# Optimization experiments

Measured on AMD Instinct MI355X. Metric: run time of the kernel, lower is better.

The kernel has to match this reference:

```python
import jax, jax.numpy as jnp
import numpy as np

N_HEADS = 16

def setup_inputs() -> dict:
    key = jax.random.key(0)
    k1, k2 = jax.random.split(key)
    B, S, H = 4, 2048, 1024
    hidden_states = jax.random.normal(k1, (B, S, H), dtype=jnp.float32)
    # F.linear weight: [out_features, in_features]; init std per module
    std = 0.02 / np.sqrt(2.0 * 24 * H)
    queries_weight = jax.random.normal(k2, (H, H), dtype=jnp.float32) * std
    return {"hidden_states": hidden_states, "queries_weight": queries_weight}


def reference(hidden_states, queries_weight):
    B, S, H = hidden_states.shape
    hd = H // N_HEADS
    # F.linear: x @ W^T
    q = hidden_states @ queries_weight.T
    qh = q.reshape(B, S, N_HEADS, hd)          # [B,S,h,d]
    xh = hidden_states.reshape(B, S, N_HEADS, hd)
    # pre_attn = Q K^T (no softmax), then attn @ V with K=V=x heads
    pre_attn = jnp.einsum('bqhd,bkhd->bhqk', qh, xh)   # [B,h,S,S]
    attn = jnp.einsum('bhqk,bkhd->bqhd', pre_attn, xh) # [B,S,h,d]
    return attn.reshape(B, S, H)
```

## Files before the change

### kernel.cpp

```cpp
#include <hip/hip_runtime.h>
#include <hip/hip_bf16.h>


typedef __bf16 bf16x8 __attribute__((ext_vector_type(8)));
typedef float f32x4 __attribute__((ext_vector_type(4)));

typedef __attribute__((address_space(3))) unsigned int lds_u32;
typedef const __attribute__((address_space(1))) unsigned int glb_u32;

__device__ __forceinline__ void gld_lds16(const void* g, void* l) {
    __builtin_amdgcn_global_load_lds((glb_u32*)g, (lds_u32*)l, 16, 0, 0);
}

__device__ __forceinline__ unsigned short f2bf(float f) {
    unsigned int u = __float_as_uint(f);
    u += 0x7FFFu + ((u >> 16) & 1u);
    return (unsigned short)(u >> 16);
}

#define XT_S 136

__global__ __launch_bounds__(256) void gx_partial(
        const float* __restrict__ x, const float* __restrict__ W,
        unsigned short* __restrict__ xb, unsigned short* __restrict__ Wb,
        float* __restrict__ Gp) {
    __shared__ __align__(16) unsigned short xt[64 * XT_S];
    const int tid = threadIdx.x;
    const int chunk = blockIdx.x;
    const int bh = blockIdx.y;
    const int fb = bh * 8 + chunk;
    const int b = bh >> 4, h = bh & 15;
    const int wave = tid >> 6, lane = tid & 63;
    const int lm = lane & 15, quad = lane >> 4;

    {
        size_t base = (size_t)fb * 2048 + (size_t)tid * 8;
        float4 v0 = *(const float4*)&W[base];
        float4 v1 = *(const float4*)&W[base + 4];
        ushort4 o0 = {f2bf(v0.x), f2bf(v0.y), f2bf(v0.z), f2bf(v0.w)};
        ushort4 o1 = {f2bf(v1.x), f2bf(v1.y), f2bf(v1.z), f2bf(v1.w)};
        *(ushort4*)&Wb[base] = o0;
        *(ushort4*)&Wb[base + 4] = o1;
    }

    f32x4 acc[4] = {};
    for (int half = 0; half < 2; ++half) {
        const size_t gbase =
            ((size_t)(b * 2048 + chunk * 256 + half * 128)) * 1024 + h * 64;
        __syncthreads();
        #pragma unroll
        for (int i = 0; i < 8; ++i) {
            int idx = tid + 256 * i;
            int s = idx >> 4;
            int c = (idx & 15) * 4;
            float4 v = *(const float4*)&x[gbase + (size_t)s * 1024 + c];
            ushort4 o = {f2bf(v.x), f2bf(v.y), f2bf(v.z), f2bf(v.w)};
            *(ushort4*)&xb[gbase + (size_t)s * 1024 + c] = o;
            xt[(c + 0) * XT_S + s] = o.x;
            xt[(c + 1) * XT_S + s] = o.y;
            xt[(c + 2) * XT_S + s] = o.z;
            xt[(c + 3) * XT_S + s] = o.w;
        }
        __syncthreads();
        #pragma unroll
        for (int k = 0; k < 4; ++k) {
            bf16x8 af = *(const bf16x8*)&xt[(wave * 16 + lm) * XT_S + k * 32 + quad * 8];
            #pragma unroll
            for (int ni = 0; ni < 4; ++ni) {
                bf16x8 bg = *(const bf16x8*)&xt[(ni * 16 + lm) * XT_S + k * 32 + quad * 8];
                acc[ni] = __builtin_amdgcn_mfma_f32_16x16x32_bf16(af, bg, acc[ni], 0, 0, 0);
            }
        }
    }
    float* gp = Gp + ((size_t)(chunk * 64 + bh)) * 4096;
    #pragma unroll
    for (int ni = 0; ni < 4; ++ni)
        #pragma unroll
        for (int r = 0; r < 4; ++r)
            gp[(wave * 16 + quad * 4 + r) * 64 + ni * 16 + lm] = acc[ni][r];
}

__global__ __launch_bounds__(256) void g_reduce(
        const float* __restrict__ Gp, unsigned short* __restrict__ Gb) {
    const int bh = blockIdx.x;
    const int e0 = blockIdx.y * 1024 + threadIdx.x * 4;
    float4 s = {0.f, 0.f, 0.f, 0.f};
    #pragma unroll
    for (int c = 0; c < 8; ++c) {
        float4 v = *(const float4*)&Gp[((size_t)(c * 64 + bh)) * 4096 + e0];
        s.x += v.x; s.y += v.y; s.z += v.z; s.w += v.w;
    }
    ushort4 o;
    o.x = f2bf(s.x); o.y = f2bf(s.y); o.z = f2bf(s.z); o.w = f2bf(s.w);
    *(ushort4*)&Gb[(size_t)bh * 4096 + e0] = o;
}

__global__ __launch_bounds__(256, 2) void gemm_qout(
        const unsigned short* __restrict__ xb, const unsigned short* __restrict__ Wb,
        const unsigned short* __restrict__ Gb, float* __restrict__ out) {
    __shared__ __align__(16) unsigned short smem[26624];
    unsigned short* lA = smem;
    unsigned short* lB = smem + 8192;
    unsigned short* Qt = smem;
    unsigned short* G2 = smem + 17408;
    const int tid = threadIdx.x;
    const int m0 = blockIdx.x * 128;
    const int n0 = blockIdx.y * 128;
    const int b  = blockIdx.x >> 4;
    const int h0 = blockIdx.y * 2;
    const int lane = tid & 63, wave = tid >> 6;
    const int wr = (wave >> 1) * 64, wc = (wave & 1) * 64;
    const int lm = lane & 15, quad = lane >> 4;
    const int srow = wave * 32 + (lane >> 3);
    const int scol = (((lane & 7) ^ ((lane >> 3) & 7))) * 8;

    #pragma unroll
    for (int i = 0; i < 4; ++i) {
        int idx = tid + 256 * i;
        int hh = idx >> 9;
        int rr = (idx >> 3) & 63;
        int cc = (idx & 7) * 8;
        *(uint4*)&G2[hh * 4608 + rr * 72 + cc] =
            *(const uint4*)&Gb[((size_t)(b * 16 + h0 + hh)) * 4096 + rr * 64 + cc];
    }

    f32x4 acc[4][4] = {};
    for (int kt = 0; kt < 1024; kt += 64) {
        const unsigned short* ga = &xb[(size_t)(m0 + srow) * 1024 + kt + scol];
        const unsigned short* gb = &Wb[(size_t)(n0 + srow) * 1024 + kt + scol];
        #pragma unroll
        for (int i = 0; i < 4; ++i) {
            gld_lds16(ga + (size_t)i * 8 * 1024, &lA[(wave * 32 + i * 8) * 64]);
            gld_lds16(gb + (size_t)i * 8 * 1024, &lB[(wave * 32 + i * 8) * 64]);
        }
        __syncthreads();
        #pragma unroll
        for (int kk = 0; kk < 2; ++kk) {
            bf16x8 af[4], bg[4];
            #pragma unroll
            for (int mi = 0; mi < 4; ++mi) {
                int ra = wr + mi * 16 + lm;
                int jb = (kk * 4 + quad) ^ (ra & 7);
                af[mi] = *(const bf16x8*)&lA[ra * 64 + jb * 8];
            }
            #pragma unroll
            for (int ni = 0; ni < 4; ++ni) {
                int rb = wc + ni * 16 + lm;
                int jb = (kk * 4 + quad) ^ (rb & 7);
                bg[ni] = *(const bf16x8*)&lB[rb * 64 + jb * 8];
            }
            #pragma unroll
            for (int mi = 0; mi < 4; ++mi)
                #pragma unroll
                for (int ni = 0; ni < 4; ++ni)
                    acc[mi][ni] = __builtin_amdgcn_mfma_f32_16x16x32_bf16(
                        af[mi], bg[ni], acc[mi][ni], 0, 0, 0);
        }
        __syncthreads();
    }
    #pragma unroll
    for (int mi = 0; mi < 4; ++mi)
        #pragma unroll
        for (int ni = 0; ni < 4; ++ni)
            #pragma unroll
            for (int r = 0; r < 4; ++r)
                Qt[(wr + mi * 16 + quad * 4 + r) * 136 + wc + ni * 16 + lm] =
                    f2bf(acc[mi][ni][r]);
    #pragma unroll
    for (int mi = 0; mi < 4; ++mi)
        #pragma unroll
        for (int ni = 0; ni < 4; ++ni)
            acc[mi][ni] = (f32x4){0.f, 0.f, 0.f, 0.f};
    const int hh = wave & 1;
    #pragma unroll
    for (int kk = 0; kk < 2; ++kk) {
        bf16x8 af[4], bg[4];
        #pragma unroll
        for (int mi = 0; mi < 4; ++mi)
            af[mi] = *(const bf16x8*)&Qt[(wr + mi * 16 + lm) * 136 + wc + kk * 32 + quad * 8];
        #pragma unroll
        for (int ni = 0; ni < 4; ++ni)
            bg[ni] = *(const bf16x8*)&G2[hh * 4608 + (ni * 16 + lm) * 72 + kk * 32 + quad * 8];
        #pragma unroll
        for (int mi = 0; mi < 4; ++mi)
            #pragma unroll
            for (int ni = 0; ni < 4; ++ni)
                acc[mi][ni] = __builtin_amdgcn_mfma_f32_16x16x32_bf16(
                    af[mi], bg[ni], acc[mi][ni], 0, 0, 0);
    }
    #pragma unroll
    for (int mi = 0; mi < 4; ++mi)
        #pragma unroll
        for (int ni = 0; ni < 4; ++ni)
            #pragma unroll
            for (int r = 0; r < 4; ++r)
                out[(size_t)(m0 + wr + mi * 16 + quad * 4 + r) * 1024
                    + n0 + wc + ni * 16 + lm] = acc[mi][ni][r];
}

extern "C" void kernel_launch(void* const* d_in, const int* in_sizes, int n_in,
                              void* d_out, int out_size, void* d_ws, size_t ws_size,
                              hipStream_t stream) {
    const float* x = (const float*)d_in[0];
    const float* W = (const float*)d_in[1];
    float* out = (float*)d_out;
    char* ws = (char*)d_ws;
    unsigned short* xb = (unsigned short*)(ws);
    unsigned short* Wb = (unsigned short*)(ws + 16777216);
    float*          Gp = (float*)        (ws + 18874368);
    unsigned short* Gb = (unsigned short*)(ws + 27262976);

    gx_partial<<<dim3(8, 64), 256, 0, stream>>>(x, W, xb, Wb, Gp);
    g_reduce<<<dim3(64, 4), 256, 0, stream>>>(Gp, Gb);
    gemm_qout<<<dim3(64, 8), 256, 0, stream>>>(xb, Wb, Gb, out);
}
```

Measured before the change: 112.9 us.

## Prefetch second x half in gx_partial and widen gemm K-tile to 128

gx_partial now loads the second 128-row half of x into registers while running MFMAs on the first half. It uses two XOR-swizzled LDS buffers in place of the padded transpose buffer, which removes one barrier and hides global latency. gemm_qout doubles its K tile to 128, halving the number of loop iterations and barriers, with a matching swizzle. Because the larger lB tile now overlaps the G2 region, the G matrix is held in registers and written to LDS only after the main loop. The cost is higher LDS use per block (64KB) and more registers, which could limit occupancy.

```diff
diff --git a/kernel.cpp b/kernel.cpp
--- a/kernel.cpp
+++ b/kernel.cpp
@@ -18,13 +18,11 @@
     return (unsigned short)(u >> 16);
 }
 
-#define XT_S 136
-
 __global__ __launch_bounds__(256) void gx_partial(
         const float* __restrict__ x, const float* __restrict__ W,
         unsigned short* __restrict__ xb, unsigned short* __restrict__ Wb,
         float* __restrict__ Gp) {
-    __shared__ __align__(16) unsigned short xt[64 * XT_S];
+    __shared__ __align__(16) unsigned short xt[2][64 * 128];
     const int tid = threadIdx.x;
     const int chunk = blockIdx.x;
     const int bh = blockIdx.y;
@@ -43,35 +41,78 @@
         *(ushort4*)&Wb[base + 4] = o1;
     }
 
+    const int sc = (tid & 15) * 4;
+    const int sr = tid >> 4;
+    const size_t gcol = (size_t)h * 64 + sc;
+    const int wsz0 = ((tid & 7) ^ 0) << 3;
+    const int wsz1 = ((tid & 7) ^ 2) << 3;
+    const int wsz2 = ((tid & 7) ^ 4) << 3;
+    const int wsz3 = ((tid & 7) ^ 6) << 3;
+    const int rA = wave * 16 + lm;
+    const int swzA = ((((rA >> 2) & 7) ^ ((rA & 3) << 1)) << 3);
+    int swzB[4];
+    #pragma unroll
+    for (int ni = 0; ni < 4; ++ni) {
+        int rb = ni * 16 + lm;
+        swzB[ni] = ((((rb >> 2) & 7) ^ ((rb & 3) << 1)) << 3);
+    }
+    const int colq = quad * 8;
+    const size_t row0 = (size_t)(b * 2048 + chunk * 256);
+
     f32x4 acc[4] = {};
-    for (int half = 0; half < 2; ++half) {
-        const size_t gbase =
-            ((size_t)(b * 2048 + chunk * 256 + half * 128)) * 1024 + h * 64;
-        __syncthreads();
-        #pragma unroll
-        for (int i = 0; i < 8; ++i) {
-            int idx = tid + 256 * i;
-            int s = idx >> 4;
-            int c = (idx & 15) * 4;
-            float4 v = *(const float4*)&x[gbase + (size_t)s * 1024 + c];
-            ushort4 o = {f2bf(v.x), f2bf(v.y), f2bf(v.z), f2bf(v.w)};
-            *(ushort4*)&xb[gbase + (size_t)s * 1024 + c] = o;
-            xt[(c + 0) * XT_S + s] = o.x;
-            xt[(c + 1) * XT_S + s] = o.y;
-            xt[(c + 2) * XT_S + s] = o.z;
-            xt[(c + 3) * XT_S + s] = o.w;
-        }
-        __syncthreads();
-        #pragma unroll
-        for (int k = 0; k < 4; ++k) {
-            bf16x8 af = *(const bf16x8*)&xt[(wave * 16 + lm) * XT_S + k * 32 + quad * 8];
-            #pragma unroll
-            for (int ni = 0; ni < 4; ++ni) {
-                bf16x8 bg = *(const bf16x8*)&xt[(ni * 16 + lm) * XT_S + k * 32 + quad * 8];
-                acc[ni] = __builtin_amdgcn_mfma_f32_16x16x32_bf16(af, bg, acc[ni], 0, 0, 0);
-            }
-        }
-    }
+    float4 v[8];
+
+    #pragma unroll
+    for (int i = 0; i < 8; ++i)
+        v[i] = *(const float4*)&x[(row0 + sr + 16 * i) * 1024 + gcol];
+    #pragma unroll
+    for (int i = 0; i < 8; ++i) {
+        int s = sr + 16 * i;
+        ushort4 o = {f2bf(v[i].x), f2bf(v[i].y), f2bf(v[i].z), f2bf(v[i].w)};
+        *(ushort4*)&xb[(row0 + s) * 1024 + gcol] = o;
+        xt[0][(sc + 0) * 128 + (s ^ wsz0)] = o.x;
+        xt[0][(sc + 1) * 128 + (s ^ wsz1)] = o.y;
+        xt[0][(sc + 2) * 128 + (s ^ wsz2)] = o.z;
+        xt[0][(sc + 3) * 128 + (s ^ wsz3)] = o.w;
+    }
+    __syncthreads();
+
+    #pragma unroll
+    for (int i = 0; i < 8; ++i)
+        v[i] = *(const float4*)&x[(row0 + 128 + sr + 16 * i) * 1024 + gcol];
+
+    #pragma unroll
+    for (int k = 0; k < 4; ++k) {
+        bf16x8 af = *(const bf16x8*)&xt[0][rA * 128 + ((k * 32 + colq) ^ swzA)];
+        #pragma unroll
+        for (int ni = 0; ni < 4; ++ni) {
+            bf16x8 bg = *(const bf16x8*)&xt[0][(ni * 16 + lm) * 128 + ((k * 32 + colq) ^ swzB[ni])];
+            acc[ni] = __builtin_amdgcn_mfma_f32_16x16x32_bf16(af, bg, acc[ni], 0, 0, 0);
+        }
+    }
+
+    #pragma unroll
+    for (int i = 0; i < 8; ++i) {
+        int s = sr + 16 * i;
+        ushort4 o = {f2bf(v[i].x), f2bf(v[i].y), f2bf(v[i].z), f2bf(v[i].w)};
+        *(ushort4*)&xb[(row0 + 128 + s) * 1024 + gcol] = o;
+        xt[1][(sc + 0) * 128 + (s ^ wsz0)] = o.x;
+        xt[1][(sc + 1) * 128 + (s ^ wsz1)] = o.y;
+        xt[1][(sc + 2) * 128 + (s ^ wsz2)] = o.z;
+        xt[1][(sc + 3) * 128 + (s ^ wsz3)] = o.w;
+    }
+    __syncthreads();
+
+    #pragma unroll
+    for (int k = 0; k < 4; ++k) {
+        bf16x8 af = *(const bf16x8*)&xt[1][rA * 128 + ((k * 32 + colq) ^ swzA)];
+        #pragma unroll
+        for (int ni = 0; ni < 4; ++ni) {
+            bf16x8 bg = *(const bf16x8*)&xt[1][(ni * 16 + lm) * 128 + ((k * 32 + colq) ^ swzB[ni])];
+            acc[ni] = __builtin_amdgcn_mfma_f32_16x16x32_bf16(af, bg, acc[ni], 0, 0, 0);
+        }
+    }
+
     float* gp = Gp + ((size_t)(chunk * 64 + bh)) * 4096;
     #pragma unroll
     for (int ni = 0; ni < 4; ++ni)
@@ -98,9 +139,9 @@
 __global__ __launch_bounds__(256, 2) void gemm_qout(
         const unsigned short* __restrict__ xb, const unsigned short* __restrict__ Wb,
         const unsigned short* __restrict__ Gb, float* __restrict__ out) {
-    __shared__ __align__(16) unsigned short smem[26624];
+    __shared__ __align__(16) unsigned short smem[32768];
     unsigned short* lA = smem;
-    unsigned short* lB = smem + 8192;
+    unsigned short* lB = smem + 16384;
     unsigned short* Qt = smem;
     unsigned short* G2 = smem + 17408;
     const int tid = threadIdx.x;
@@ -111,43 +152,43 @@
     const int lane = tid & 63, wave = tid >> 6;
     const int wr = (wave >> 1) * 64, wc = (wave & 1) * 64;
     const int lm = lane & 15, quad = lane >> 4;
-    const int srow = wave * 32 + (lane >> 3);
-    const int scol = (((lane & 7) ^ ((lane >> 3) & 7))) * 8;
-
+
+    uint4 gr[4];
     #pragma unroll
     for (int i = 0; i < 4; ++i) {
         int idx = tid + 256 * i;
         int hh = idx >> 9;
         int rr = (idx >> 3) & 63;
         int cc = (idx & 7) * 8;
-        *(uint4*)&G2[hh * 4608 + rr * 72 + cc] =
-            *(const uint4*)&Gb[((size_t)(b * 16 + h0 + hh)) * 4096 + rr * 64 + cc];
+        gr[i] = *(const uint4*)&Gb[((size_t)(b * 16 + h0 + hh)) * 4096 + rr * 64 + cc];
     }
 
     f32x4 acc[4][4] = {};
-    for (int kt = 0; kt < 1024; kt += 64) {
-        const unsigned short* ga = &xb[(size_t)(m0 + srow) * 1024 + kt + scol];
-        const unsigned short* gb = &Wb[(size_t)(n0 + srow) * 1024 + kt + scol];
-        #pragma unroll
-        for (int i = 0; i < 4; ++i) {
-            gld_lds16(ga + (size_t)i * 8 * 1024, &lA[(wave * 32 + i * 8) * 64]);
-            gld_lds16(gb + (size_t)i * 8 * 1024, &lB[(wave * 32 + i * 8) * 64]);
+    for (int kt = 0; kt < 1024; kt += 128) {
+        #pragma unroll
+        for (int i = 0; i < 8; ++i) {
+            int rloc = wave * 32 + i * 4 + (lane >> 4);
+            int jsrc = ((lane & 15) ^ (rloc & 7)) * 8;
+            gld_lds16(&xb[(size_t)(m0 + rloc) * 1024 + kt + jsrc],
+                      &lA[(wave * 32 + i * 4) * 128]);
+            gld_lds16(&Wb[(size_t)(n0 + rloc) * 1024 + kt + jsrc],
+                      &lB[(wave * 32 + i * 4) * 128]);
         }
         __syncthreads();
         #pragma unroll
-        for (int kk = 0; kk < 2; ++kk) {
+        for (int kk = 0; kk < 4; ++kk) {
             bf16x8 af[4], bg[4];
             #pragma unroll
             for (int mi = 0; mi < 4; ++mi) {
                 int ra = wr + mi * 16 + lm;
                 int jb = (kk * 4 + quad) ^ (ra & 7);
-                af[mi] = *(const bf16x8*)&lA[ra * 64 + jb * 8];
+                af[mi] = *(const bf16x8*)&lA[ra * 128 + jb * 8];
             }
             #pragma unroll
             for (int ni = 0; ni < 4; ++ni) {
                 int rb = wc + ni * 16 + lm;
                 int jb = (kk * 4 + quad) ^ (rb & 7);
-                bg[ni] = *(const bf16x8*)&lB[rb * 64 + jb * 8];
+                bg[ni] = *(const bf16x8*)&lB[rb * 128 + jb * 8];
             }
             #pragma unroll
             for (int mi = 0; mi < 4; ++mi)
@@ -166,6 +207,15 @@
             for (int r = 0; r < 4; ++r)
                 Qt[(wr + mi * 16 + quad * 4 + r) * 136 + wc + ni * 16 + lm] =
                     f2bf(acc[mi][ni][r]);
+    #pragma unroll
+    for (int i = 0; i < 4; ++i) {
+        int idx = tid + 256 * i;
+        int hh = idx >> 9;
+        int rr = (idx >> 3) & 63;
+        int cc = (idx & 7) * 8;
+        *(uint4*)&G2[hh * 4608 + rr * 72 + cc] = gr[i];
+    }
+    __syncthreads();
     #pragma unroll
     for (int mi = 0; mi < 4; ++mi)
         #pragma unroll
```

New measurement: 121.1 us. 7.3% more time.

## Split bf16 conversion into standalone kernel and parallelize Gram partials over more chunks

Applied to the files above, without the earlier changes.

The fused convert-and-Gram kernel becomes two kernels. One is a flat, fully parallel fp32-to-bf16 conversion of x and W. The other is a Gram-partial kernel that reads bf16 x, uses 16 chunks of 128 rows instead of 8 chunks of 256, and transposes into an XOR-swizzled LDS layout to avoid bank conflicts. This raises parallelism in the Gram stage (1024 blocks instead of 512) and lets conversion run at full bandwidth. In exchange it adds a kernel launch, re-reads xb from global memory, and doubles the partial sums the reduce kernel must add.

```diff
diff --git a/kernel.cpp b/kernel.cpp
--- a/kernel.cpp
+++ b/kernel.cpp
@@ -18,61 +18,74 @@
     return (unsigned short)(u >> 16);
 }
 
-#define XT_S 136
-
-__global__ __launch_bounds__(256) void gx_partial(
+__global__ __launch_bounds__(256) void convert_bf16(
         const float* __restrict__ x, const float* __restrict__ W,
-        unsigned short* __restrict__ xb, unsigned short* __restrict__ Wb,
-        float* __restrict__ Gp) {
-    __shared__ __align__(16) unsigned short xt[64 * XT_S];
+        unsigned short* __restrict__ xb, unsigned short* __restrict__ Wb) {
+    const int bid = blockIdx.x;
+    const float* src;
+    unsigned short* dst;
+    size_t base;
+    if (bid < 4096) { src = x; dst = xb; base = (size_t)bid * 2048; }
+    else            { src = W; dst = Wb; base = (size_t)(bid - 4096) * 2048; }
+    const size_t idx = base + (size_t)threadIdx.x * 8;
+    float4 v0 = *(const float4*)&src[idx];
+    float4 v1 = *(const float4*)&src[idx + 4];
+    ushort4 o0 = {f2bf(v0.x), f2bf(v0.y), f2bf(v0.z), f2bf(v0.w)};
+    ushort4 o1 = {f2bf(v1.x), f2bf(v1.y), f2bf(v1.z), f2bf(v1.w)};
+    *(ushort4*)&dst[idx] = o0;
+    *(ushort4*)&dst[idx + 4] = o1;
+}
+
+__global__ __launch_bounds__(256) void g_partial(
+        const unsigned short* __restrict__ xb, float* __restrict__ Gp) {
+    __shared__ __align__(16) unsigned short xt[64 * 128];
+    const int c = blockIdx.x;
+    const int bh = blockIdx.y;
+    const int b = bh >> 4, h = bh & 15;
     const int tid = threadIdx.x;
-    const int chunk = blockIdx.x;
-    const int bh = blockIdx.y;
-    const int fb = bh * 8 + chunk;
-    const int b = bh >> 4, h = bh & 15;
     const int wave = tid >> 6, lane = tid & 63;
     const int lm = lane & 15, quad = lane >> 4;
 
-    {
-        size_t base = (size_t)fb * 2048 + (size_t)tid * 8;
-        float4 v0 = *(const float4*)&W[base];
-        float4 v1 = *(const float4*)&W[base + 4];
-        ushort4 o0 = {f2bf(v0.x), f2bf(v0.y), f2bf(v0.z), f2bf(v0.w)};
-        ushort4 o1 = {f2bf(v1.x), f2bf(v1.y), f2bf(v1.z), f2bf(v1.w)};
-        *(ushort4*)&Wb[base] = o0;
-        *(ushort4*)&Wb[base + 4] = o1;
-    }
-
+    const size_t gbase = ((size_t)(b * 2048 + c * 128)) * 1024 + h * 64;
+    const int lrow = tid >> 3;
+    const int lseg = (tid & 7) * 8;
+    bf16x8 rv[4];
+    #pragma unroll
+    for (int i = 0; i < 4; ++i)
+        rv[i] = *(const bf16x8*)&xb[gbase + (size_t)(lrow + 32 * i) * 1024 + lseg];
+
+    #pragma unroll
+    for (int i = 0; i < 4; ++i) {
+        int s = lrow + 32 * i;
+        #pragma unroll
+        for (int j = 0; j < 8; ++j) {
+            int d = lseg + j;
+            int g = ((d >> 2) & 7) ^ ((d & 3) << 1);
+            xt[d * 128 + (s ^ (g << 3))] = ((const unsigned short*)&rv[i])[j];
+        }
+    }
+    __syncthreads();
+
+    const int rA = wave * 16 + lm;
+    const int swzA = ((((rA >> 2) & 7) ^ ((rA & 3) << 1)) << 3);
+    int swzB[4];
+    #pragma unroll
+    for (int ni = 0; ni < 4; ++ni) {
+        int rb = ni * 16 + lm;
+        swzB[ni] = ((((rb >> 2) & 7) ^ ((rb & 3) << 1)) << 3);
+    }
+    const int colq = quad * 8;
     f32x4 acc[4] = {};
-    for (int half = 0; half < 2; ++half) {
-        const size_t gbase =
-            ((size_t)(b * 2048 + chunk * 256 + half * 128)) * 1024 + h * 64;
-        __syncthreads();
-        #pragma unroll
-        for (int i = 0; i < 8; ++i) {
-            int idx = tid + 256 * i;
-            int s = idx >> 4;
-            int c = (idx & 15) * 4;
-            float4 v = *(const float4*)&x[gbase + (size_t)s * 1024 + c];
-            ushort4 o = {f2bf(v.x), f2bf(v.y), f2bf(v.z), f2bf(v.w)};
-            *(ushort4*)&xb[gbase + (size_t)s * 1024 + c] = o;
-            xt[(c + 0) * XT_S + s] = o.x;
-            xt[(c + 1) * XT_S + s] = o.y;
-            xt[(c + 2) * XT_S + s] = o.z;
-            xt[(c + 3) * XT_S + s] = o.w;
-        }
-        __syncthreads();
-        #pragma unroll
-        for (int k = 0; k < 4; ++k) {
-            bf16x8 af = *(const bf16x8*)&xt[(wave * 16 + lm) * XT_S + k * 32 + quad * 8];
-            #pragma unroll
-            for (int ni = 0; ni < 4; ++ni) {
-                bf16x8 bg = *(const bf16x8*)&xt[(ni * 16 + lm) * XT_S + k * 32 + quad * 8];
-                acc[ni] = __builtin_amdgcn_mfma_f32_16x16x32_bf16(af, bg, acc[ni], 0, 0, 0);
-            }
-        }
-    }
-    float* gp = Gp + ((size_t)(chunk * 64 + bh)) * 4096;
+    #pragma unroll
+    for (int k = 0; k < 4; ++k) {
+        bf16x8 af = *(const bf16x8*)&xt[rA * 128 + ((k * 32 + colq) ^ swzA)];
+        #pragma unroll
+        for (int ni = 0; ni < 4; ++ni) {
+            bf16x8 bg = *(const bf16x8*)&xt[(ni * 16 + lm) * 128 + ((k * 32 + colq) ^ swzB[ni])];
+            acc[ni] = __builtin_amdgcn_mfma_f32_16x16x32_bf16(af, bg, acc[ni], 0, 0, 0);
+        }
+    }
+    float* gp = Gp + ((size_t)(c * 64 + bh)) * 4096;
     #pragma unroll
     for (int ni = 0; ni < 4; ++ni)
         #pragma unroll
@@ -86,7 +99,7 @@
     const int e0 = blockIdx.y * 1024 + threadIdx.x * 4;
     float4 s = {0.f, 0.f, 0.f, 0.f};
     #pragma unroll
-    for (int c = 0; c < 8; ++c) {
+    for (int c = 0; c < 16; ++c) {
         float4 v = *(const float4*)&Gp[((size_t)(c * 64 + bh)) * 4096 + e0];
         s.x += v.x; s.y += v.y; s.z += v.z; s.w += v.w;
     }
@@ -208,9 +221,10 @@
     unsigned short* xb = (unsigned short*)(ws);
     unsigned short* Wb = (unsigned short*)(ws + 16777216);
     float*          Gp = (float*)        (ws + 18874368);
-    unsigned short* Gb = (unsigned short*)(ws + 27262976);
-
-    gx_partial<<<dim3(8, 64), 256, 0, stream>>>(x, W, xb, Wb, Gp);
+    unsigned short* Gb = (unsigned short*)(ws + 35651584);
+
+    convert_bf16<<<dim3(4608), 256, 0, stream>>>(x, W, xb, Wb);
+    g_partial<<<dim3(16, 64), 256, 0, stream>>>(xb, Gp);
     g_reduce<<<dim3(64, 4), 256, 0, stream>>>(Gp, Gb);
     gemm_qout<<<dim3(64, 8), 256, 0, stream>>>(xb, Wb, Gb, out);
 }
```

New measurement: 116.5 us. +3.2%, slower.
